# Kernel optimization log

Measured on AMD Instinct MI355X. Metric: run time of the kernel, lower is better.

The kernel has to match this reference:

```python
import jax, jax.numpy as jnp
import numpy as np

B, L, D_MODEL = 2, 2048, 1024
D_INNER, D_STATE, DT_RANK, D_CONV = 2048, 16, 64, 4
EPS = 1e-5


def setup_inputs() -> dict:
    key = jax.random.key(0)
    ks = jax.random.split(key, 12)
    s = lambda fan: 1.0 / np.sqrt(fan)
    return {
        "x": jax.random.normal(ks[0], (B, L, D_MODEL), jnp.float32),
        "norm_w": jnp.ones((D_MODEL,), jnp.float32),
        "W_in": jax.random.normal(ks[1], (2 * D_INNER, D_MODEL), jnp.float32) * s(D_MODEL),
        "W_conv": jax.random.normal(ks[2], (D_INNER, D_CONV), jnp.float32) * s(D_CONV),
        "b_conv": jnp.zeros((D_INNER,), jnp.float32),
        "W_xproj": jax.random.normal(ks[3], (DT_RANK + 2 * D_STATE, D_INNER), jnp.float32) * s(D_INNER),
        "W_dt": jax.random.normal(ks[4], (D_INNER, DT_RANK), jnp.float32) * s(DT_RANK),
        "b_dt": jax.random.normal(ks[5], (D_INNER,), jnp.float32) * 0.1,
        # A initialized as log(1..d_state) per channel (standard Mamba S4D-real init)
        "A_log": jnp.log(jnp.broadcast_to(jnp.arange(1, D_STATE + 1, dtype=jnp.float32), (D_INNER, D_STATE))),
        "D": jnp.ones((D_INNER,), jnp.float32),
        "W_out": jax.random.normal(ks[6], (D_MODEL, D_INNER), jnp.float32) * s(D_INNER),
    }


def _mamba_residual(x, norm_w, W_in, W_conv, b_conv, W_xproj, W_dt, b_dt, A_log, D, W_out):
    # RMSNorm
    xn = x * jax.lax.rsqrt(jnp.mean(x * x, axis=-1, keepdims=True) + EPS) * norm_w
    # in_proj -> split into u (ssm branch) and z (gate)
    xz = jnp.einsum("bld,ed->ble", xn, W_in)            # [b, l, 2*d_inner]
    u, z = jnp.split(xz, 2, axis=-1)                     # each [b, l, d_inner]
    # depthwise causal conv1d over time
    u_t = jnp.transpose(u, (0, 2, 1))                    # [b, d_inner, l]
    u_c = jax.lax.conv_general_dilated(
        u_t, W_conv[:, None, :], window_strides=(1,),
        padding=[(D_CONV - 1, 0)], feature_group_count=D_INNER,
        dimension_numbers=("NCH", "OIH", "NCH"))
    u_c = jax.nn.silu(u_c + b_conv[None, :, None])       # [b, d_inner, l]
    u = jnp.transpose(u_c, (0, 2, 1))                    # [b, l, d_inner]
    # x_proj -> (dt, B, C)
    x_dbl = jnp.einsum("bld,ed->ble", u, W_xproj)        # [b, l, dt_rank+2n]
    dt, Bm, Cm = jnp.split(x_dbl, [DT_RANK, DT_RANK + D_STATE], axis=-1)
    dt = jax.nn.softplus(jnp.einsum("blr,dr->bld", dt, W_dt) + b_dt)  # [b, l, d_inner]
    A = -jnp.exp(A_log)                                  # [d_inner, n]

    # selective scan over time
    def step(h, ins):
        dt_t, B_t, C_t, u_t = ins                        # [b,d],[b,n],[b,n],[b,d]
        dA = jnp.exp(dt_t[..., None] * A)                # [b, d, n]
        h = dA * h + (dt_t * u_t)[..., None] * B_t[:, None, :]
        y = jnp.einsum("bdn,bn->bd", h, C_t)
        return h, y

    h0 = jnp.zeros((x.shape[0], D_INNER, D_STATE), x.dtype)
    ins = (jnp.transpose(dt, (1, 0, 2)), jnp.transpose(Bm, (1, 0, 2)),
           jnp.transpose(Cm, (1, 0, 2)), jnp.transpose(u, (1, 0, 2)))
    _, ys = jax.lax.scan(step, h0, ins)                  # [l, b, d_inner]
    y = jnp.transpose(ys, (1, 0, 2)) + u * D             # [b, l, d_inner]
    y = y * jax.nn.silu(z)
    out = jnp.einsum("ble,de->bld", y, W_out)
    return out + x  # residual (block_mode 'residual'/'none')


def reference(x, norm_w, W_in, W_conv, b_conv, W_xproj, W_dt, b_dt, A_log, D, W_out):
    return _mamba_residual(x, norm_w, W_in, W_conv, b_conv, W_xproj, W_dt, b_dt, A_log, D, W_out)
```

## Files before the change

### kernel.cpp

```cpp
#include <hip/hip_runtime.h>

typedef unsigned short u16;
typedef unsigned int u32;
typedef short bf16x8 __attribute__((ext_vector_type(8)));
typedef float f32x4 __attribute__((ext_vector_type(4)));

static constexpr int LS = 2048;
static constexpr int DM = 1024;
static constexpr int DI = 2048;
static constexpr int DSn = 16;
static constexpr int DTRk = 64;
static constexpr int MR = 4096;
static constexpr int NCH = 64;
static constexpr int CL = LS / NCH;
static constexpr float L2E = 1.44269504f;

#define DEV __device__ __forceinline__

DEV u16 f2bf(float f) {
  u32 u = __float_as_uint(f);
  u32 r = (u + 0x7FFF + ((u >> 16) & 1)) >> 16;
  return (u16)r;
}
DEV float bf2f(u16 h) { return __uint_as_float(((u32)h) << 16); }

DEV void gload16(const u16* g, u16* l) {
  __builtin_amdgcn_global_load_lds((const __attribute__((address_space(1))) u32*)g,
                                   (__attribute__((address_space(3))) u32*)l, 16, 0, 0);
}

DEV void bar() { asm volatile("s_barrier" ::: "memory"); }

#define CALC_POWERS(dst, basev)                                              \
  do {                                                                       \
    const float e1_ = (basev);                                               \
    const float e2_ = e1_ * e1_, e3_ = e2_ * e1_, e4_ = e2_ * e2_;           \
    const float e5_ = e4_ * e1_, e6_ = e4_ * e2_, e7_ = e4_ * e3_,           \
                e8_ = e4_ * e4_;                                             \
    dst[0] = e1_; dst[1] = e2_; dst[2] = e3_; dst[3] = e4_;                  \
    dst[4] = e5_; dst[5] = e6_; dst[6] = e7_; dst[7] = e8_;                  \
    dst[8] = e8_ * e1_;  dst[9] = e8_ * e2_;  dst[10] = e8_ * e3_;           \
    dst[11] = e8_ * e4_; dst[12] = e8_ * e5_; dst[13] = e8_ * e6_;           \
    dst[14] = e8_ * e7_; dst[15] = e8_ * e8_;                                \
  } while (0)

__global__ __launch_bounds__(256) void cvt_weights(const float* __restrict__ W_in,
                                                   const float* __restrict__ W_out,
                                                   const float* __restrict__ W_dt,
                                                   const float* __restrict__ W_xp,
                                                   u16* __restrict__ Win_b,
                                                   u16* __restrict__ Wout_b,
                                                   u16* __restrict__ Wdt_b,
                                                   u16* __restrict__ Wxp_b) {
  const int N0 = 4096 * 1024;
  const int N1 = N0 + 1024 * 2048;
  const int N2 = N1 + 2048 * 64;
  const int N3 = N2 + 128 * 2048;
  int i = blockIdx.x * 256 + threadIdx.x;
  const int stride = gridDim.x * 256;
  for (; i < N3; i += stride) {
    if (i < N0) {
      Win_b[i] = f2bf(W_in[i]);
    } else if (i < N1) {
      const int j = i - N0; Wout_b[j] = f2bf(W_out[j]);
    } else if (i < N2) {
      const int j = i - N1; Wdt_b[j] = f2bf(W_dt[j]);
    } else {
      const int j = i - N2; const int r = j >> 11, c = j & 2047;
      Wxp_b[j] = (r < 96) ? f2bf(W_xp[r * 2048 + c]) : (u16)0;
    }
  }
}

__global__ __launch_bounds__(256) void rmsnorm_kernel(const float* __restrict__ x,
                                                      const float* __restrict__ w,
                                                      u16* __restrict__ xn) {
  const int row = blockIdx.x;
  const int tid = threadIdx.x;
  const float4 v = reinterpret_cast<const float4*>(x + (size_t)row * DM)[tid];
  float ss = v.x * v.x + v.y * v.y + v.z * v.z + v.w * v.w;
#pragma unroll
  for (int o = 32; o; o >>= 1) ss += __shfl_xor(ss, o);
  __shared__ float red[4];
  if ((tid & 63) == 0) red[tid >> 6] = ss;
  __syncthreads();
  const float tot = red[0] + red[1] + red[2] + red[3];
  const float scale = rsqrtf(tot * (1.0f / DM) + 1e-5f);
  const float4 wv = reinterpret_cast<const float4*>(w)[tid];
  ushort4 o4;
  o4.x = f2bf(v.x * scale * wv.x);
  o4.y = f2bf(v.y * scale * wv.y);
  o4.z = f2bf(v.z * scale * wv.z);
  o4.w = f2bf(v.w * scale * wv.w);
  *reinterpret_cast<ushort4*>(&xn[(size_t)row * DM + tid * 4]) = o4;
}

DEV void stage_op(const u16* __restrict__ P, int K, int rowbase, int k0,
                  u16* dst, int tid) {
#pragma unroll
  for (int i = 0; i < 4; ++i) {
    const int row = i * 64 + (tid >> 3);
    const int slot = (tid & 7) ^ (row & 7);
    gload16(P + (size_t)(rowbase + row) * K + k0 + slot * 8, dst + i * 4096 + tid * 8);
  }
}

#define ISS_A(dst, off, MH) do { \
  _Pragma("unroll") for (int m_ = 0; m_ < 4; ++m_) \
  _Pragma("unroll") for (int kk_ = 0; kk_ < 2; ++kk_) \
    dst[m_ * 2 + kk_] = *reinterpret_cast<const bf16x8*>( \
        &SL[(off) + wr * 8192 + ((MH) * 64 + m_ * 16 + lrow) * 64 + ((kk_ * 4 + kq) ^ rsw) * 8]); \
} while (0)

#define ISS_B(dst, off, NH) do { \
  _Pragma("unroll") for (int n_ = 0; n_ < 2; ++n_) \
  _Pragma("unroll") for (int kk_ = 0; kk_ < 2; ++kk_) \
    dst[n_ * 2 + kk_] = *reinterpret_cast<const bf16x8*>( \
        &SL[(off) + 16384 + bh * 8192 + (bq * 64 + ((NH) * 2 + n_) * 16 + lrow) * 64 + ((kk_ * 4 + kq) ^ rsw) * 8]); \
} while (0)

#define MMAQ(areg, breg, MH, NH) do { \
  __builtin_amdgcn_s_setprio(1); \
  _Pragma("unroll") for (int m_ = 0; m_ < 4; ++m_) \
  _Pragma("unroll") for (int n_ = 0; n_ < 2; ++n_) \
  _Pragma("unroll") for (int kk_ = 0; kk_ < 2; ++kk_) \
    acc[(MH) * 4 + m_][(NH) * 2 + n_] = __builtin_amdgcn_mfma_f32_16x16x32_bf16( \
        areg[m_ * 2 + kk_], breg[n_ * 2 + kk_], acc[(MH) * 4 + m_][(NH) * 2 + n_], 0, 0, 0); \
  __builtin_amdgcn_s_setprio(0); \
} while (0)

template <int EPI>
__global__ __launch_bounds__(512, 2) void gemm256(const u16* __restrict__ A,
                                                  const u16* __restrict__ Bw,
                                                  int M, int N, int K, int Klen,
                                                  u16* __restrict__ outB,
                                                  float* __restrict__ outF) {
  __shared__ __align__(16) u16 SL[2 * 32768];
  const int tid = threadIdx.x;
  const int lane = tid & 63;
  const int wid = tid >> 6;
  const int wr = wid >> 2;
  const int wc = wid & 3;
  const int lrow = lane & 15;
  const int kq = lane >> 4;
  const int rsw = lane & 7;
  const int bh = wc >> 1, bq = wc & 1;

  const int nwg = gridDim.x * gridDim.y;
  int wg = blockIdx.y * gridDim.x + blockIdx.x;
  wg = (wg & 7) * (nwg >> 3) + (wg >> 3);
  const int bn = (wg % gridDim.x) * 256;
  const int bm = (wg / gridDim.x) * 256;
  const int koff = blockIdx.z * Klen;

  const int nt = Klen >> 6;

  f32x4 acc[8][4] = {};
  bf16x8 a0[8], a1[8], b0[4], b1[4];

  stage_op(A, K, bm, koff, &SL[0], tid);
  stage_op(Bw, K, bn, koff, &SL[16384], tid);
  asm volatile("s_waitcnt vmcnt(0)" ::: "memory");
  bar();

  for (int t = 0; t < nt; ++t) {
    const int cs = (t & 1) * 32768;
    const int ns = ((t + 1) & 1) * 32768;
    if (t + 1 < nt) {
      stage_op(A, K, bm, koff + (t + 1) * 64, &SL[ns], tid);
      stage_op(Bw, K, bn, koff + (t + 1) * 64, &SL[ns + 16384], tid);
    }
    ISS_A(a0, cs, 0);
    ISS_B(b0, cs, 0);
    MMAQ(a0, b0, 0, 0);
    ISS_B(b1, cs, 1);
    MMAQ(a0, b1, 0, 1);
    ISS_A(a1, cs, 1);
    MMAQ(a1, b0, 1, 0);
    MMAQ(a1, b1, 1, 1);
    if (t + 1 < nt) {
      asm volatile("s_waitcnt vmcnt(0)" ::: "memory");
      bar();
    }
  }

  if (EPI == 0) {
#pragma unroll
    for (int m = 0; m < 8; ++m)
#pragma unroll
      for (int n = 0; n < 4; ++n) {
        const int col = bn + wc * 64 + n * 16 + lrow;
#pragma unroll
        for (int rr = 0; rr < 4; ++rr) {
          const int row = bm + wr * 128 + m * 16 + kq * 4 + rr;
          outB[(size_t)row * N + col] = f2bf(acc[m][n][rr]);
        }
      }
  } else {
    float* dstF = outF + (size_t)blockIdx.z * MR * N;
#pragma unroll
    for (int m = 0; m < 8; ++m)
#pragma unroll
      for (int n = 0; n < 4; ++n) {
        const int col = bn + wc * 64 + n * 16 + lrow;
#pragma unroll
        for (int rr = 0; rr < 4; ++rr) {
          const int row = bm + wr * 128 + m * 16 + kq * 4 + rr;
          dstF[(size_t)row * N + col] = acc[m][n][rr];
        }
      }
  }
}

__global__ __launch_bounds__(256) void outproj_reduce4(const float* __restrict__ p,
                                                       const float* __restrict__ x,
                                                       float* __restrict__ out) {
  const int id = blockIdx.x * 256 + threadIdx.x;
  float4 o = reinterpret_cast<const float4*>(x)[id];
#pragma unroll
  for (int s = 0; s < 4; ++s) {
    const float4 a = reinterpret_cast<const float4*>(p + (size_t)s * MR * 1024)[id];
    o.x += a.x; o.y += a.y; o.z += a.z; o.w += a.w;
  }
  reinterpret_cast<float4*>(out)[id] = o;
}

__global__ __launch_bounds__(256) void gemm_dt(const u16* __restrict__ A,
                                               const u16* __restrict__ Bw,
                                               int M, int N, int K,
                                               u16* __restrict__ outB,
                                               const float* __restrict__ aux) {
  __shared__ __align__(16) u16 As[128 * 32];
  __shared__ __align__(16) u16 Bs[128 * 32];
  const int tid = threadIdx.x;
  const int lane = tid & 63;
  const int wid = tid >> 6;
  const int wr = wid >> 1, wc = wid & 1;
  const int nwg = gridDim.x * gridDim.y;
  int wg = blockIdx.y * gridDim.x + blockIdx.x;
  wg = (wg & 7) * (nwg >> 3) + (wg >> 3);
  const int bn = (wg % gridDim.x) * 128;
  const int bm = (wg / gridDim.x) * 128;
  const int r0 = tid >> 2;
  const int c0 = (tid & 3) * 8;
  const int lrow = lane & 15, kq = lane >> 4;

  f32x4 acc[4][4] = {};

  const u16* Ab = A + (size_t)bm * K;
  const u16* Bb = Bw + (size_t)bn * K;

  for (int k0 = 0; k0 < K; k0 += 32) {
    gload16(Ab + (size_t)r0 * K + k0 + c0, &As[r0 * 32 + c0]);
    gload16(Ab + (size_t)(r0 + 64) * K + k0 + c0, &As[(r0 + 64) * 32 + c0]);
    gload16(Bb + (size_t)r0 * K + k0 + c0, &Bs[r0 * 32 + c0]);
    gload16(Bb + (size_t)(r0 + 64) * K + k0 + c0, &Bs[(r0 + 64) * 32 + c0]);
    __syncthreads();
    bf16x8 af[4], bfr[4];
#pragma unroll
    for (int m = 0; m < 4; ++m)
      af[m] = *reinterpret_cast<const bf16x8*>(&As[(wr * 64 + m * 16 + lrow) * 32 + kq * 8]);
#pragma unroll
    for (int n = 0; n < 4; ++n)
      bfr[n] = *reinterpret_cast<const bf16x8*>(&Bs[(wc * 64 + n * 16 + lrow) * 32 + kq * 8]);
#pragma unroll
    for (int m = 0; m < 4; ++m)
#pragma unroll
      for (int n = 0; n < 4; ++n)
        acc[m][n] = __builtin_amdgcn_mfma_f32_16x16x32_bf16(af[m], bfr[n], acc[m][n], 0, 0, 0);
    __syncthreads();
  }

#pragma unroll
  for (int m = 0; m < 4; ++m) {
#pragma unroll
    for (int n = 0; n < 4; ++n) {
      const int col = bn + wc * 64 + n * 16 + lrow;
#pragma unroll
      for (int r = 0; r < 4; ++r) {
        const int row = bm + wr * 64 + m * 16 + kq * 4 + r;
        const float xv = acc[m][n][r] + aux[col];
        const float sp = fmaxf(xv, 0.f) + log1pf(__expf(-fabsf(xv)));
        outB[(size_t)row * N + col] = f2bf(sp);
      }
    }
  }
}

__global__ __launch_bounds__(256) void gemm_xproj_splitk(const u16* __restrict__ A,
                                                         const u16* __restrict__ Bw,
                                                         float* __restrict__ p0,
                                                         float* __restrict__ p1) {
  __shared__ __align__(16) u16 As[128 * 32];
  __shared__ __align__(16) u16 Bs[128 * 32];
  const int tid = threadIdx.x;
  const int lane = tid & 63;
  const int wid = tid >> 6;
  const int wr = wid >> 1, wc = wid & 1;
  const int kp = blockIdx.x;
  const int bm = blockIdx.y * 128;
  const int koff = kp * 256;
  const int r0 = tid >> 2;
  const int c0 = (tid & 3) * 8;
  const int lrow = lane & 15, kq = lane >> 4;

  f32x4 acc[4][4] = {};
  const u16* Ab = A + (size_t)bm * DI + koff;
  const u16* Bb = Bw + koff;

  for (int k0 = 0; k0 < 256; k0 += 32) {
    gload16(Ab + (size_t)r0 * DI + k0 + c0, &As[r0 * 32 + c0]);
    gload16(Ab + (size_t)(r0 + 64) * DI + k0 + c0, &As[(r0 + 64) * 32 + c0]);
    gload16(Bb + (size_t)r0 * DI + k0 + c0, &Bs[r0 * 32 + c0]);
    gload16(Bb + (size_t)(r0 + 64) * DI + k0 + c0, &Bs[(r0 + 64) * 32 + c0]);
    __syncthreads();
    bf16x8 af[4], bfr[4];
#pragma unroll
    for (int m = 0; m < 4; ++m)
      af[m] = *reinterpret_cast<const bf16x8*>(&As[(wr * 64 + m * 16 + lrow) * 32 + kq * 8]);
#pragma unroll
    for (int n = 0; n < 4; ++n)
      bfr[n] = *reinterpret_cast<const bf16x8*>(&Bs[(wc * 64 + n * 16 + lrow) * 32 + kq * 8]);
#pragma unroll
    for (int m = 0; m < 4; ++m)
#pragma unroll
      for (int n = 0; n < 4; ++n)
        acc[m][n] = __builtin_amdgcn_mfma_f32_16x16x32_bf16(af[m], bfr[n], acc[m][n], 0, 0, 0);
    __syncthreads();
  }

  float* dst = (kp < 4 ? p0 : p1) + (size_t)(kp & 3) * MR * 128;
#pragma unroll
  for (int m = 0; m < 4; ++m)
#pragma unroll
    for (int n = 0; n < 4; ++n) {
      const int col = wc * 64 + n * 16 + lrow;
#pragma unroll
      for (int r = 0; r < 4; ++r) {
        const int row = bm + wr * 64 + m * 16 + kq * 4 + r;
        dst[(size_t)row * 128 + col] = acc[m][n][r];
      }
    }
}

__global__ __launch_bounds__(256) void xproj_reduce(const float* __restrict__ p0,
                                                    const float* __restrict__ p1,
                                                    float* __restrict__ xdbl,
                                                    u16* __restrict__ dtr) {
  const int id = blockIdx.x * 256 + threadIdx.x;
  const int row = id >> 7, col = id & 127;
  float s = 0.f;
#pragma unroll
  for (int kp = 0; kp < 4; ++kp) s += p0[(size_t)kp * MR * 128 + id];
#pragma unroll
  for (int kp = 0; kp < 4; ++kp) s += p1[(size_t)kp * MR * 128 + id];
  if (col < 96) xdbl[(size_t)row * 96 + col] = s;
  if (col < 64) dtr[(size_t)row * 64 + col] = f2bf(s);
}

__global__ __launch_bounds__(256) void conv_silu_kernel(const u16* __restrict__ xz,
                                                        const float* __restrict__ Wc,
                                                        const float* __restrict__ bc,
                                                        u16* __restrict__ uc) {
  const int id = blockIdx.x * 256 + threadIdx.x;
  const int d8 = id & (DI / 8 - 1);
  const int t = (id >> 8) & (LS - 1);
  const int b = id >> 19;
  const int d0 = d8 * 8;
  const size_t rowb = (size_t)b * LS;
  bf16x8 r[4];
#pragma unroll
  for (int k = 0; k < 4; ++k) {
    const int tt = t - 3 + k;
    if (tt >= 0)
      r[k] = *reinterpret_cast<const bf16x8*>(&xz[(rowb + tt) * (2 * DI) + d0]);
    else
      r[k] = bf16x8{0, 0, 0, 0, 0, 0, 0, 0};
  }
  const float4 bc0 = *reinterpret_cast<const float4*>(&bc[d0]);
  const float4 bc1 = *reinterpret_cast<const float4*>(&bc[d0 + 4]);
  const float bcv[8] = {bc0.x, bc0.y, bc0.z, bc0.w, bc1.x, bc1.y, bc1.z, bc1.w};
  u16 o[8];
#pragma unroll
  for (int j = 0; j < 8; ++j) {
    const float4 w = *reinterpret_cast<const float4*>(&Wc[(d0 + j) * 4]);
    float s = bcv[j];
    s += bf2f((u16)r[0][j]) * w.x;
    s += bf2f((u16)r[1][j]) * w.y;
    s += bf2f((u16)r[2][j]) * w.z;
    s += bf2f((u16)r[3][j]) * w.w;
    const float sl = s / (1.f + __expf(-s));
    o[j] = f2bf(sl);
  }
  *reinterpret_cast<bf16x8*>(&uc[(rowb + t) * DI + d0]) =
      *reinterpret_cast<const bf16x8*>(o);
}


__global__ __launch_bounds__(128, 4) void scan_phase1(const u16* __restrict__ dtb,
                                                      const float* __restrict__ xdbl,
                                                      const u16* __restrict__ uc,
                                                      const float* __restrict__ Alog,
                                                      float* __restrict__ P,
                                                      float* __restrict__ S) {
  __shared__ __align__(16) u16 s_dt[16 * 128];
  __shared__ __align__(16) u16 s_uc[16 * 128];
  __shared__ __align__(16) float s_b[16 * 16];
  const int tid = threadIdx.x;
  const int blk = blockIdx.x;
  const int d0 = (blk & 15) * 128;
  const int c = (blk >> 4) & (NCH - 1);
  const int b = blk >> 10;
  const int d = d0 + tid;
  const size_t tbase = (size_t)b * LS + c * CL;

  float Av[16];
  bool fastA = true;
#pragma unroll
  for (int j = 0; j < 16; j += 4) {
    const float4 Alv = *reinterpret_cast<const float4*>(&Alog[d * DSn + j]);
    Av[j + 0] = -__expf(Alv.x); Av[j + 1] = -__expf(Alv.y);
    Av[j + 2] = -__expf(Alv.z); Av[j + 3] = -__expf(Alv.w);
  }
#pragma unroll
  for (int j = 0; j < 16; ++j)
    fastA = fastA && (fabsf(Av[j] + (float)(j + 1)) < 1e-3f * (float)(j + 1));

  float h[16];
#pragma unroll
  for (int j = 0; j < 16; ++j) h[j] = 0.f;
  float sdt = 0.f;

  for (int w = 0; w < 2; ++w) {
    const size_t twb = tbase + w * 16;
#pragma unroll
    for (int j = 0; j < 2; ++j) {
      const int k = j * 128 + tid;
      const int row = k >> 4, col = (k & 15) * 8;
      gload16(dtb + (twb + row) * DI + d0 + col, &s_dt[row * 128 + col]);
      gload16(uc + (twb + row) * DI + d0 + col, &s_uc[row * 128 + col]);
    }
    if (tid < 64) {
      gload16((const u16*)(xdbl + (twb + (tid >> 2)) * 96 + DTRk + (tid & 3) * 4),
              (u16*)&s_b[tid * 4]);
    }
    __syncthreads();
    if (fastA) {
      for (int tr = 0; tr < 16; ++tr) {
        const float dtv = bf2f(s_dt[tr * 128 + tid]);
        const float uv = bf2f(s_uc[tr * 128 + tid]);
        const float du = dtv * uv;
        sdt += dtv;
        float dA[16];
        CALC_POWERS(dA, exp2f(-L2E * dtv));
        float Bf[16];
#pragma unroll
        for (int j = 0; j < 16; j += 4) {
          const float4 Bv = *reinterpret_cast<const float4*>(&s_b[tr * 16 + j]);
          Bf[j] = Bv.x; Bf[j + 1] = Bv.y; Bf[j + 2] = Bv.z; Bf[j + 3] = Bv.w;
        }
#pragma unroll
        for (int j = 0; j < 16; ++j) h[j] = dA[j] * h[j] + du * Bf[j];
      }
    } else {
      for (int tr = 0; tr < 16; ++tr) {
        const float dtv = bf2f(s_dt[tr * 128 + tid]);
        const float uv = bf2f(s_uc[tr * 128 + tid]);
        const float du = dtv * uv;
        sdt += dtv;
        float Bf[16];
#pragma unroll
        for (int j = 0; j < 16; j += 4) {
          const float4 Bv = *reinterpret_cast<const float4*>(&s_b[tr * 16 + j]);
          Bf[j] = Bv.x; Bf[j + 1] = Bv.y; Bf[j + 2] = Bv.z; Bf[j + 3] = Bv.w;
        }
#pragma unroll
        for (int j = 0; j < 16; ++j)
          h[j] = exp2f(dtv * Av[j] * L2E) * h[j] + du * Bf[j];
      }
    }
    __syncthreads();
  }

  const size_t oi = (((size_t)b * NCH + c) * DI + d) * DSn;
  float Pw[16];
  if (fastA) {
    CALC_POWERS(Pw, exp2f(-L2E * sdt));
  } else {
#pragma unroll
    for (int j = 0; j < 16; ++j) Pw[j] = exp2f(Av[j] * L2E * sdt);
  }
#pragma unroll
  for (int j = 0; j < 16; j += 4) {
    float4 Sv = {h[j], h[j + 1], h[j + 2], h[j + 3]};
    float4 Pv = {Pw[j], Pw[j + 1], Pw[j + 2], Pw[j + 3]};
    *reinterpret_cast<float4*>(&S[oi + j]) = Sv;
    *reinterpret_cast<float4*>(&P[oi + j]) = Pv;
  }
}

__global__ __launch_bounds__(256) void scan_phase2(const float* __restrict__ P,
                                                   float* __restrict__ S) {
  const int gid = blockIdx.x * 256 + threadIdx.x;
  const int ng = gid & 3;
  const int d = (gid >> 2) & (DI - 1);
  const int b = gid >> 13;
  float4 h = {0.f, 0.f, 0.f, 0.f};
  for (int cc = 0; cc < NCH; ++cc) {
    const size_t oi = (((size_t)b * NCH + cc) * DI + d) * DSn + ng * 4;
    const float4 Pv = *reinterpret_cast<const float4*>(&P[oi]);
    const float4 Sv = *reinterpret_cast<const float4*>(&S[oi]);
    *reinterpret_cast<float4*>(&S[oi]) = h;
    h.x = Sv.x + Pv.x * h.x;
    h.y = Sv.y + Pv.y * h.y;
    h.z = Sv.z + Pv.z * h.z;
    h.w = Sv.w + Pv.w * h.w;
  }
}

__global__ __launch_bounds__(128, 4) void scan_phase3(const u16* __restrict__ dtb,
                                                      const float* __restrict__ xdbl,
                                                      const u16* __restrict__ uc,
                                                      const u16* __restrict__ xz,
                                                      const float* __restrict__ Alog,
                                                      const float* __restrict__ Dp,
                                                      const float* __restrict__ Hin,
                                                      u16* __restrict__ yb) {
  __shared__ __align__(16) u16 s_dt[16 * 128];
  __shared__ __align__(16) u16 s_uc[16 * 128];
  __shared__ __align__(16) u16 s_z[16 * 128];
  __shared__ __align__(16) float s_bc[16 * 32];
  const int tid = threadIdx.x;
  const int blk = blockIdx.x;
  const int d0 = (blk & 15) * 128;
  const int c = (blk >> 4) & (NCH - 1);
  const int b = blk >> 10;
  const int d = d0 + tid;
  const size_t tbase = (size_t)b * LS + c * CL;

  float Av[16];
  bool fastA = true;
#pragma unroll
  for (int j = 0; j < 16; j += 4) {
    const float4 Alv = *reinterpret_cast<const float4*>(&Alog[d * DSn + j]);
    Av[j + 0] = -__expf(Alv.x); Av[j + 1] = -__expf(Alv.y);
    Av[j + 2] = -__expf(Alv.z); Av[j + 3] = -__expf(Alv.w);
  }
#pragma unroll
  for (int j = 0; j < 16; ++j)
    fastA = fastA && (fabsf(Av[j] + (float)(j + 1)) < 1e-3f * (float)(j + 1));

  const float Dd = Dp[d];
  const size_t oi = (((size_t)b * NCH + c) * DI + d) * DSn;
  float h[16];
#pragma unroll
  for (int j = 0; j < 16; j += 4) {
    const float4 hv = *reinterpret_cast<const float4*>(&Hin[oi + j]);
    h[j] = hv.x; h[j + 1] = hv.y; h[j + 2] = hv.z; h[j + 3] = hv.w;
  }

  for (int w = 0; w < 2; ++w) {
    const size_t twb = tbase + w * 16;
#pragma unroll
    for (int j = 0; j < 2; ++j) {
      const int k = j * 128 + tid;
      const int row = k >> 4, col = (k & 15) * 8;
      gload16(dtb + (twb + row) * DI + d0 + col, &s_dt[row * 128 + col]);
      gload16(uc + (twb + row) * DI + d0 + col, &s_uc[row * 128 + col]);
      gload16(xz + (twb + row) * (2 * DI) + DI + d0 + col, &s_z[row * 128 + col]);
    }
    {
      gload16((const u16*)(xdbl + (twb + (tid >> 3)) * 96 + DTRk + (tid & 7) * 4),
              (u16*)&s_bc[tid * 4]);
    }
    __syncthreads();
#define P3_STEP(DA_STMT)                                                        \
    for (int tr = 0; tr < 16; ++tr) {                                           \
      const float dtv = bf2f(s_dt[tr * 128 + tid]);                             \
      const float uv = bf2f(s_uc[tr * 128 + tid]);                              \
      const float du = dtv * uv;                                                \
      float dA[16];                                                             \
      DA_STMT;                                                                  \
      float Bf[16], Cf[16];                                                     \
      _Pragma("unroll")                                                         \
      for (int j = 0; j < 16; j += 4) {                                         \
        const float4 Bv = *reinterpret_cast<const float4*>(&s_bc[tr * 32 + j]); \
        const float4 Cv = *reinterpret_cast<const float4*>(&s_bc[tr * 32 + 16 + j]); \
        Bf[j] = Bv.x; Bf[j + 1] = Bv.y; Bf[j + 2] = Bv.z; Bf[j + 3] = Bv.w;     \
        Cf[j] = Cv.x; Cf[j + 1] = Cv.y; Cf[j + 2] = Cv.z; Cf[j + 3] = Cv.w;     \
      }                                                                         \
      _Pragma("unroll")                                                         \
      for (int j = 0; j < 16; ++j) h[j] = dA[j] * h[j] + du * Bf[j];            \
      float y0 = 0.f, y1 = 0.f, y2 = 0.f, y3 = 0.f;                             \
      _Pragma("unroll")                                                         \
      for (int j = 0; j < 16; j += 4) {                                         \
        y0 += h[j] * Cf[j];                                                     \
        y1 += h[j + 1] * Cf[j + 1];                                             \
        y2 += h[j + 2] * Cf[j + 2];                                             \
        y3 += h[j + 3] * Cf[j + 3];                                             \
      }                                                                         \
      const float y = (y0 + y1) + (y2 + y3) + uv * Dd;                          \
      const float z = bf2f(s_z[tr * 128 + tid]);                                \
      const float sz = z / (1.f + __expf(-z));                                  \
      yb[(twb + tr) * DI + d] = f2bf(y * sz);                                   \
    }
    if (fastA) {
      P3_STEP(CALC_POWERS(dA, exp2f(-L2E * dtv)));
    } else {
      P3_STEP({ _Pragma("unroll") for (int j = 0; j < 16; ++j) dA[j] = exp2f(dtv * Av[j] * L2E); });
    }
#undef P3_STEP
    __syncthreads();
  }
}

extern "C" void kernel_launch(void* const* d_in, const int* in_sizes, int n_in,
                              void* d_out, int out_size, void* d_ws, size_t ws_size,
                              hipStream_t stream) {
  (void)in_sizes; (void)n_in; (void)out_size; (void)ws_size;
  const float* x      = (const float*)d_in[0];
  const float* norm_w = (const float*)d_in[1];
  const float* W_in   = (const float*)d_in[2];
  const float* W_conv = (const float*)d_in[3];
  const float* b_conv = (const float*)d_in[4];
  const float* W_xp   = (const float*)d_in[5];
  const float* W_dt   = (const float*)d_in[6];
  const float* b_dt   = (const float*)d_in[7];
  const float* A_log  = (const float*)d_in[8];
  const float* Dvec   = (const float*)d_in[9];
  const float* W_out  = (const float*)d_in[10];
  float* out = (float*)d_out;

  char* ws = (char*)d_ws;
  size_t off = 0;
  auto alloc = [&](size_t bytes) -> void* {
    void* p = ws + off;
    off += (bytes + 255) & ~(size_t)255;
    return p;
  };
  u16* Win_b  = (u16*)alloc((size_t)4096 * 1024 * 2);
  u16* Wout_b = (u16*)alloc((size_t)1024 * 2048 * 2);
  u16* Wxp_b  = (u16*)alloc((size_t)128 * 2048 * 2);
  u16* Wdt_b  = (u16*)alloc((size_t)2048 * 64 * 2);
  u16* xn_b   = (u16*)alloc((size_t)MR * DM * 2);
  u16* xz_b   = (u16*)alloc((size_t)MR * 2 * DI * 2);
  u16* uc_b   = (u16*)alloc((size_t)MR * DI * 2);
  float* xdbl = (float*)alloc((size_t)MR * 96 * 4);
  u16* dtr_b  = (u16*)alloc((size_t)MR * 64 * 2);
  u16* dtf_b  = (u16*)alloc((size_t)MR * DI * 2);
  u16* y_b    = (u16*)alloc((size_t)MR * DI * 2);
  float* Sbuf = (float*)alloc((size_t)2 * NCH * DI * DSn * 4);
  float* part0 = (float*)Win_b;
  float* part1 = (float*)xn_b;
  float* Pbuf = (float*)y_b;
  float* opart = (float*)xz_b;

  cvt_weights<<<2048, 256, 0, stream>>>(W_in, W_out, W_dt, W_xp,
                                        Win_b, Wout_b, Wdt_b, Wxp_b);

  rmsnorm_kernel<<<MR, 256, 0, stream>>>(x, norm_w, xn_b);

  gemm256<0><<<dim3(16, 16, 1), 512, 0, stream>>>(xn_b, Win_b, MR, 4096, 1024, 1024,
                                                  xz_b, nullptr);
  conv_silu_kernel<<<4096, 256, 0, stream>>>(xz_b, W_conv, b_conv, uc_b);
  gemm_xproj_splitk<<<dim3(8, 32), 256, 0, stream>>>(uc_b, Wxp_b, part0, part1);
  xproj_reduce<<<2048, 256, 0, stream>>>(part0, part1, xdbl, dtr_b);
  gemm_dt<<<dim3(16, 32), 256, 0, stream>>>(dtr_b, Wdt_b, MR, 2048, 64, dtf_b, b_dt);
  scan_phase1<<<2048, 128, 0, stream>>>(dtf_b, xdbl, uc_b, A_log, Pbuf, Sbuf);
  scan_phase2<<<64, 256, 0, stream>>>(Pbuf, Sbuf);
  scan_phase3<<<2048, 128, 0, stream>>>(dtf_b, xdbl, uc_b, xz_b, A_log, Dvec,
                                        Sbuf, y_b);
  gemm256<1><<<dim3(4, 16, 4), 512, 0, stream>>>(y_b, Wout_b, MR, 1024, 2048, 512,
                                                 nullptr, opart);
  outproj_reduce4<<<4096, 256, 0, stream>>>(opart, x, out);
}
```

Before: 227.4 us.

## Shrink GEMM tiles to 128x256 with K=32 steps and higher occupancy

Replaces the 256x256, K=64 GEMM tile with a 128x256, K=32 tile. LDS drops from 128KB to 48KB and launch bounds allow 4 blocks per CU. Both the in_proj and out_proj launches double their grid. The goal is more concurrent waves and more blocks to hide load latency, at the cost of less data reuse per tile, twice as many barriers per unit of K, and a new swizzle pattern.

```diff
diff --git a/kernel.cpp b/kernel.cpp
--- a/kernel.cpp
+++ b/kernel.cpp
@@ -95,47 +95,13 @@
   *reinterpret_cast<ushort4*>(&xn[(size_t)row * DM + tid * 4]) = o4;
 }
 
-DEV void stage_op(const u16* __restrict__ P, int K, int rowbase, int k0,
-                  u16* dst, int tid) {
-#pragma unroll
-  for (int i = 0; i < 4; ++i) {
-    const int row = i * 64 + (tid >> 3);
-    const int slot = (tid & 7) ^ (row & 7);
-    gload16(P + (size_t)(rowbase + row) * K + k0 + slot * 8, dst + i * 4096 + tid * 8);
-  }
-}
-
-#define ISS_A(dst, off, MH) do { \
-  _Pragma("unroll") for (int m_ = 0; m_ < 4; ++m_) \
-  _Pragma("unroll") for (int kk_ = 0; kk_ < 2; ++kk_) \
-    dst[m_ * 2 + kk_] = *reinterpret_cast<const bf16x8*>( \
-        &SL[(off) + wr * 8192 + ((MH) * 64 + m_ * 16 + lrow) * 64 + ((kk_ * 4 + kq) ^ rsw) * 8]); \
-} while (0)
-
-#define ISS_B(dst, off, NH) do { \
-  _Pragma("unroll") for (int n_ = 0; n_ < 2; ++n_) \
-  _Pragma("unroll") for (int kk_ = 0; kk_ < 2; ++kk_) \
-    dst[n_ * 2 + kk_] = *reinterpret_cast<const bf16x8*>( \
-        &SL[(off) + 16384 + bh * 8192 + (bq * 64 + ((NH) * 2 + n_) * 16 + lrow) * 64 + ((kk_ * 4 + kq) ^ rsw) * 8]); \
-} while (0)
-
-#define MMAQ(areg, breg, MH, NH) do { \
-  __builtin_amdgcn_s_setprio(1); \
-  _Pragma("unroll") for (int m_ = 0; m_ < 4; ++m_) \
-  _Pragma("unroll") for (int n_ = 0; n_ < 2; ++n_) \
-  _Pragma("unroll") for (int kk_ = 0; kk_ < 2; ++kk_) \
-    acc[(MH) * 4 + m_][(NH) * 2 + n_] = __builtin_amdgcn_mfma_f32_16x16x32_bf16( \
-        areg[m_ * 2 + kk_], breg[n_ * 2 + kk_], acc[(MH) * 4 + m_][(NH) * 2 + n_], 0, 0, 0); \
-  __builtin_amdgcn_s_setprio(0); \
-} while (0)
-
 template <int EPI>
-__global__ __launch_bounds__(512, 2) void gemm256(const u16* __restrict__ A,
-                                                  const u16* __restrict__ Bw,
-                                                  int M, int N, int K, int Klen,
-                                                  u16* __restrict__ outB,
-                                                  float* __restrict__ outF) {
-  __shared__ __align__(16) u16 SL[2 * 32768];
+__global__ __launch_bounds__(512, 4) void gemm128n256(const u16* __restrict__ A,
+                                                      const u16* __restrict__ Bw,
+                                                      int M, int N, int K, int Klen,
+                                                      u16* __restrict__ outB,
+                                                      float* __restrict__ outF) {
+  __shared__ __align__(16) u16 SL[2 * 12288];
   const int tid = threadIdx.x;
   const int lane = tid & 63;
   const int wid = tid >> 6;
@@ -143,69 +109,89 @@
   const int wc = wid & 3;
   const int lrow = lane & 15;
   const int kq = lane >> 4;
-  const int rsw = lane & 7;
-  const int bh = wc >> 1, bq = wc & 1;
 
   const int nwg = gridDim.x * gridDim.y;
   int wg = blockIdx.y * gridDim.x + blockIdx.x;
   wg = (wg & 7) * (nwg >> 3) + (wg >> 3);
   const int bn = (wg % gridDim.x) * 256;
-  const int bm = (wg / gridDim.x) * 256;
+  const int bm = (wg / gridDim.x) * 128;
   const int koff = blockIdx.z * Klen;
 
-  const int nt = Klen >> 6;
-
-  f32x4 acc[8][4] = {};
-  bf16x8 a0[8], a1[8], b0[4], b1[4];
-
-  stage_op(A, K, bm, koff, &SL[0], tid);
-  stage_op(Bw, K, bn, koff, &SL[16384], tid);
+  const int nt = Klen >> 5;
+
+  f32x4 acc[4][4] = {};
+  bf16x8 a[4], b[4];
+
+  const int srA = tid >> 2;
+  const int slA = (tid & 3) ^ ((srA >> 1) & 3);
+  const int srB0 = tid >> 2, srB1 = 128 + (tid >> 2);
+  const int slB0 = (tid & 3) ^ ((srB0 >> 1) & 3);
+  const int slB1 = (tid & 3) ^ ((srB1 >> 1) & 3);
+
+#define STAGE_TILE(ktile, sup)                                                          \
+  do {                                                                                  \
+    const int k0_ = koff + (ktile) * 32;                                                \
+    gload16(A + (size_t)(bm + srA) * K + k0_ + slA * 8, &SL[(sup) + tid * 8]);          \
+    gload16(Bw + (size_t)(bn + srB0) * K + k0_ + slB0 * 8, &SL[(sup) + 4096 + tid * 8]);\
+    gload16(Bw + (size_t)(bn + srB1) * K + k0_ + slB1 * 8, &SL[(sup) + 8192 + tid * 8]);\
+  } while (0)
+
+  STAGE_TILE(0, 0);
   asm volatile("s_waitcnt vmcnt(0)" ::: "memory");
   bar();
 
   for (int t = 0; t < nt; ++t) {
-    const int cs = (t & 1) * 32768;
-    const int ns = ((t + 1) & 1) * 32768;
-    if (t + 1 < nt) {
-      stage_op(A, K, bm, koff + (t + 1) * 64, &SL[ns], tid);
-      stage_op(Bw, K, bn, koff + (t + 1) * 64, &SL[ns + 16384], tid);
-    }
-    ISS_A(a0, cs, 0);
-    ISS_B(b0, cs, 0);
-    MMAQ(a0, b0, 0, 0);
-    ISS_B(b1, cs, 1);
-    MMAQ(a0, b1, 0, 1);
-    ISS_A(a1, cs, 1);
-    MMAQ(a1, b0, 1, 0);
-    MMAQ(a1, b1, 1, 1);
+    const int cs = (t & 1) * 12288;
+    const int ns = ((t + 1) & 1) * 12288;
+    if (t + 1 < nt) STAGE_TILE(t + 1, ns);
+#pragma unroll
+    for (int m = 0; m < 4; ++m) {
+      const int row = wr * 64 + m * 16 + lrow;
+      a[m] = *reinterpret_cast<const bf16x8*>(
+          &SL[cs + row * 32 + (kq ^ ((row >> 1) & 3)) * 8]);
+    }
+#pragma unroll
+    for (int n = 0; n < 4; ++n) {
+      const int row = wc * 64 + n * 16 + lrow;
+      b[n] = *reinterpret_cast<const bf16x8*>(
+          &SL[cs + 4096 + row * 32 + (kq ^ ((row >> 1) & 3)) * 8]);
+    }
+    __builtin_amdgcn_s_setprio(1);
+#pragma unroll
+    for (int m = 0; m < 4; ++m)
+#pragma unroll
+      for (int n = 0; n < 4; ++n)
+        acc[m][n] = __builtin_amdgcn_mfma_f32_16x16x32_bf16(a[m], b[n], acc[m][n], 0, 0, 0);
+    __builtin_amdgcn_s_setprio(0);
     if (t + 1 < nt) {
       asm volatile("s_waitcnt vmcnt(0)" ::: "memory");
       bar();
     }
   }
+#undef STAGE_TILE
 
   if (EPI == 0) {
 #pragma unroll
-    for (int m = 0; m < 8; ++m)
+    for (int m = 0; m < 4; ++m)
 #pragma unroll
       for (int n = 0; n < 4; ++n) {
         const int col = bn + wc * 64 + n * 16 + lrow;
 #pragma unroll
         for (int rr = 0; rr < 4; ++rr) {
-          const int row = bm + wr * 128 + m * 16 + kq * 4 + rr;
+          const int row = bm + wr * 64 + m * 16 + kq * 4 + rr;
           outB[(size_t)row * N + col] = f2bf(acc[m][n][rr]);
         }
       }
   } else {
     float* dstF = outF + (size_t)blockIdx.z * MR * N;
 #pragma unroll
-    for (int m = 0; m < 8; ++m)
+    for (int m = 0; m < 4; ++m)
 #pragma unroll
       for (int n = 0; n < 4; ++n) {
         const int col = bn + wc * 64 + n * 16 + lrow;
 #pragma unroll
         for (int rr = 0; rr < 4; ++rr) {
-          const int row = bm + wr * 128 + m * 16 + kq * 4 + rr;
+          const int row = bm + wr * 64 + m * 16 + kq * 4 + rr;
           dstF[(size_t)row * N + col] = acc[m][n][rr];
         }
       }
@@ -660,8 +646,8 @@
 
   rmsnorm_kernel<<<MR, 256, 0, stream>>>(x, norm_w, xn_b);
 
-  gemm256<0><<<dim3(16, 16, 1), 512, 0, stream>>>(xn_b, Win_b, MR, 4096, 1024, 1024,
-                                                  xz_b, nullptr);
+  gemm128n256<0><<<dim3(16, 32, 1), 512, 0, stream>>>(xn_b, Win_b, MR, 4096, 1024, 1024,
+                                                      xz_b, nullptr);
   conv_silu_kernel<<<4096, 256, 0, stream>>>(xz_b, W_conv, b_conv, uc_b);
   gemm_xproj_splitk<<<dim3(8, 32), 256, 0, stream>>>(uc_b, Wxp_b, part0, part1);
   xproj_reduce<<<2048, 256, 0, stream>>>(part0, part1, xdbl, dtr_b);
@@ -670,7 +656,7 @@
   scan_phase2<<<64, 256, 0, stream>>>(Pbuf, Sbuf);
   scan_phase3<<<2048, 128, 0, stream>>>(dtf_b, xdbl, uc_b, xz_b, A_log, Dvec,
                                         Sbuf, y_b);
-  gemm256<1><<<dim3(4, 16, 4), 512, 0, stream>>>(y_b, Wout_b, MR, 1024, 2048, 512,
-                                                 nullptr, opart);
+  gemm128n256<1><<<dim3(4, 32, 4), 512, 0, stream>>>(y_b, Wout_b, MR, 1024, 2048, 512,
+                                                     nullptr, opart);
   outproj_reduce4<<<4096, 256, 0, stream>>>(opart, x, out);
 }
```

Result: no change. 230.8 us (+1.5%).
